# Kernel tuning notes

Hardware: AMD Instinct MI355X
Metric: run time of the kernel (lower is better)

Reference implementation:

```python
import jax, jax.numpy as jnp
import numpy as np
from jax import lax

B, C, H, W = 4, 256, 64, 64
C8 = C // 8


def _conv1x1(x, w, b):
    # x: (B,C,H,W), w: (O,C) -> (B,O,H,W)
    return jnp.einsum('bchw,oc->bohw', x, w) + b[None, :, None, None]


def setup_inputs() -> dict:
    key = jax.random.key(0)
    ks = jax.random.split(key, 9)
    s1 = 1.0 / np.sqrt(C)          # fan-in scale for 1x1 convs
    sf = 1.0 / np.sqrt(2 * C * 9)  # fan-in scale for 3x3 conv
    return {
        'front_x':     jax.random.normal(ks[0], (B, C, H, W), jnp.float32),
        'cross_x':     jax.random.normal(ks[1], (B, C, H, W), jnp.float32),
        'front_x_hat': jax.random.normal(ks[2], (B, C, H, W), jnp.float32),
        'Wq': jax.random.normal(ks[3], (C8, C), jnp.float32) * s1,
        'bq': jnp.zeros((C8,), jnp.float32),
        'Wk': jax.random.normal(ks[4], (C8, C), jnp.float32) * s1,
        'bk': jnp.zeros((C8,), jnp.float32),
        'Wv': jax.random.normal(ks[5], (C, C), jnp.float32) * s1,
        'bv': jnp.zeros((C,), jnp.float32),
        'Wf': jax.random.normal(ks[6], (C, 2 * C, 3, 3), jnp.float32) * sf,
        'bf': jnp.zeros((C,), jnp.float32),
    }


def reference(front_x, cross_x, front_x_hat, Wq, bq, Wk, bk, Wv, bv, Wf, bf):
    b, c, h, w = front_x.shape
    hw = h * w
    # projections -> (B, C/8, HW)
    q = _conv1x1(cross_x, Wq, bq).reshape(b, -1, hw)
    k = _conv1x1(front_x, Wk, bk).reshape(b, -1, hw)
    # energy[b,i,j] = <key_i, query_j>  (B, HW, HW)
    energy = jnp.einsum('bci,bcj->bij', k, q)
    front_star = jnp.max(energy, axis=1)     # (B, HW) best key score per query
    front_arg = jnp.argmax(energy, axis=1)   # (B, HW) best key index per query
    # value projection and hard gather of best-matching value per position
    v = _conv1x1(front_x_hat, Wv, bv).reshape(b, c, hw)
    T = jnp.take_along_axis(v, front_arg[:, None, :], axis=2).reshape(b, c, h, w)
    S = front_star.reshape(b, 1, h, w)
    cat = jnp.concatenate([front_x, T], axis=1)  # (B, 2C, H, W)
    res = lax.conv_general_dilated(
        cat, Wf, window_strides=(1, 1), padding='SAME',
        dimension_numbers=('NCHW', 'OIHW', 'NCHW')) + bf[None, :, None, None]
    return front_x + res * S
```

## Files before the change

### kernel.cpp

```cpp
#include <hip/hip_runtime.h>

#define Bn 4
#define Cn 256
#define C8 32
#define Hn 64
#define Wn 64
#define HWn 4096
#define PADR 80
#define ROWS (HWn + 2 * PADR)
#define MARGIN 6e-3f

typedef __bf16 bf16x8 __attribute__((ext_vector_type(8)));
typedef float floatx4 __attribute__((ext_vector_type(4)));
typedef unsigned short u16x8 __attribute__((ext_vector_type(8)));

__device__ __forceinline__ unsigned short f2bf(float f) {
  union { float f; unsigned int u; } c; c.f = f;
  unsigned int u = c.u;
  return (unsigned short)((u + 0x7FFFu + ((u >> 16) & 1u)) >> 16);
}
__device__ __forceinline__ float bf2f(unsigned short h) {
  union { unsigned int u; float f; } c; c.u = ((unsigned int)h) << 16;
  return c.f;
}
__device__ __forceinline__ void gl_lds16(const void* g, void* l) {
  __builtin_amdgcn_global_load_lds(
      (__attribute__((address_space(1))) void*)(uintptr_t)g,
      (__attribute__((address_space(3))) void*)(uintptr_t)l, 16, 0, 0);
}

__global__ void prep_w(const float* __restrict__ Wq, const float* __restrict__ Wk,
                       const float* __restrict__ Wv, const float* __restrict__ Wf,
                       float* __restrict__ Wqf, float* __restrict__ Wkf,
                       unsigned short* __restrict__ Wvb, unsigned short* __restrict__ Wfb,
                       int* __restrict__ cnt) {
  size_t t = (size_t)blockIdx.x * 256 + threadIdx.x;
  if (t == 0) cnt[0] = 0;
  if (t < 8192) {
    int o = (int)(t / 256), c = (int)(t % 256);
    Wqf[(size_t)c * 32 + o] = Wq[t];
    Wkf[(size_t)c * 32 + o] = Wk[t];
  }
  if (t < 65536) Wvb[t] = f2bf(Wv[t]);
  if (t < (size_t)9 * 256 * 512) {
    int tap = (int)(t / (256 * 512));
    int rem = (int)(t % (256 * 512));
    int o = rem / 512, ci = rem % 512;
    Wfb[t] = f2bf(Wf[((size_t)o * 512 + ci) * 9 + tap]);
  }
}

__global__ __launch_bounds__(1024) void proj_qk(
    const float* __restrict__ cross_x, const float* __restrict__ front_x,
    const float* __restrict__ Wqf, const float* __restrict__ bq,
    const float* __restrict__ Wkf, const float* __restrict__ bk,
    float* __restrict__ qf, float* __restrict__ kf,
    unsigned short* __restrict__ qhi, unsigned short* __restrict__ qlo,
    unsigned short* __restrict__ khi, unsigned short* __restrict__ klo) {
  int tid = threadIdx.x;
  int lane = tid & 63, wv = tid >> 6;
  int slice = wv & 3;
  int chunk = wv >> 2;
  int j = blockIdx.x * 64 + lane;
  int b = blockIdx.y;
  int z = blockIdx.z;
  const float* x = (z == 0) ? cross_x : front_x;
  const float* Wg = (z == 0) ? Wqf : Wkf;
  const float* bd = (z == 0) ? bq : bk;
  float* outp = (z == 0) ? qf : kf;
  unsigned short* hip_ = (z == 0) ? qhi : khi;
  unsigned short* lop_ = (z == 0) ? qlo : klo;
  int o0 = slice * 8;
  int c0 = chunk * 64;

  __shared__ __align__(16) float Wl[8192];
  __shared__ float part[3 * 4 * 8 * 64];

  for (int u = tid; u < 8192; u += 1024) Wl[u] = Wg[u];
  __syncthreads();

  const float* xb = x + (size_t)b * Cn * HWn + j;
  floatx4 a0 = (floatx4)0.0f, a1 = (floatx4)0.0f;
#pragma unroll 16
  for (int c = c0; c < c0 + 64; ++c) {
    float xv = xb[(size_t)c * HWn];
    floatx4 wa = *reinterpret_cast<const floatx4*>(&Wl[c * 32 + o0]);
    floatx4 wb = *reinterpret_cast<const floatx4*>(&Wl[c * 32 + o0 + 4]);
    a0 += wa * xv;
    a1 += wb * xv;
  }
  if (chunk > 0) {
    float* dst = &part[(((chunk - 1) * 4 + slice) * 8) * 64];
#pragma unroll
    for (int o = 0; o < 4; ++o) { dst[o * 64 + lane] = a0[o]; dst[(o + 4) * 64 + lane] = a1[o]; }
  }
  __syncthreads();
  if (chunk != 0) return;
#pragma unroll
  for (int q = 0; q < 3; ++q) {
    const float* src = &part[((q * 4 + slice) * 8) * 64];
#pragma unroll
    for (int o = 0; o < 4; ++o) { a0[o] += src[o * 64 + lane]; a1[o] += src[(o + 4) * 64 + lane]; }
  }
  float acc[8];
#pragma unroll
  for (int o = 0; o < 4; ++o) { acc[o] = a0[o] + bd[o0 + o]; acc[o + 4] = a1[o] + bd[o0 + 4 + o]; }

  float* op = outp + ((size_t)b * HWn + j) * C8 + o0;
  u16x8 hv, lv;
#pragma unroll
  for (int o = 0; o < 8; ++o) {
    op[o] = acc[o];
    unsigned short h = f2bf(acc[o]);
    hv[o] = h;
    lv[o] = f2bf(acc[o] - bf2f(h));
  }
  *reinterpret_cast<u16x8*>(hip_ + ((size_t)b * HWn + j) * C8 + o0) = hv;
  *reinterpret_cast<u16x8*>(lop_ + ((size_t)b * HWn + j) * C8 + o0) = lv;
}

__global__ __launch_bounds__(1024) void energy_approx(
    const unsigned short* __restrict__ khi, const unsigned short* __restrict__ klo,
    const unsigned short* __restrict__ qhi, const unsigned short* __restrict__ qlo,
    float* __restrict__ star, int* __restrict__ argb,
    int* __restrict__ cnt, int* __restrict__ list) {
  int b = blockIdx.y;
  int j0 = blockIdx.x * 32;
  int tid = threadIdx.x;
  int lane = tid & 63, wv = tid >> 6;
  int lm = lane & 15, lq = lane >> 4;

  __shared__ float bv1S[16][32];
  __shared__ int   bi1S[16][32];
  __shared__ float bv2S[16][32];

  bf16x8 qh[2], ql[2];
#pragma unroll
  for (int s = 0; s < 2; ++s) {
    int j = j0 + s * 16 + lm;
    qh[s] = *reinterpret_cast<const bf16x8*>(qhi + ((size_t)b * HWn + j) * 32 + lq * 8);
    ql[s] = *reinterpret_cast<const bf16x8*>(qlo + ((size_t)b * HWn + j) * 32 + lq * 8);
  }
  const unsigned short* kh_base = khi + (size_t)b * HWn * 32 + lq * 8;
  const unsigned short* kl_base = klo + (size_t)b * HWn * 32 + lq * 8;

  float b1[2], b2[2];
#pragma unroll
  for (int s = 0; s < 2; ++s) { b1[s] = -3.0e38f; b2[s] = -3.0e38f; }

  int ibase = wv * 256;
#pragma unroll 4
  for (int it = 0; it < 16; ++it) {
    int i0 = ibase + it * 16;
    bf16x8 ah = *reinterpret_cast<const bf16x8*>(kh_base + (size_t)(i0 + lm) * 32);
    bf16x8 al = *reinterpret_cast<const bf16x8*>(kl_base + (size_t)(i0 + lm) * 32);
#pragma unroll
    for (int s = 0; s < 2; ++s) {
      floatx4 acc = (floatx4)0.0f;
      acc = __builtin_amdgcn_mfma_f32_16x16x32_bf16(ah, qh[s], acc, 0, 0, 0);
      acc = __builtin_amdgcn_mfma_f32_16x16x32_bf16(ah, ql[s], acc, 0, 0, 0);
      acc = __builtin_amdgcn_mfma_f32_16x16x32_bf16(al, qh[s], acc, 0, 0, 0);
#pragma unroll
      for (int r = 0; r < 4; ++r) {
        unsigned code = (unsigned)(it * 4 + r);
        union { float f; unsigned u; } cv; cv.f = acc[r];
        cv.u = (cv.u & ~63u) | code;
        float vp = cv.f;
        b2[s] = __builtin_amdgcn_fmed3f(vp, b1[s], b2[s]);
        b1[s] = fmaxf(b1[s], vp);
      }
    }
  }
  int i1[2];
#pragma unroll
  for (int s = 0; s < 2; ++s) {
    union { float f; unsigned u; } cv; cv.f = b1[s];
    unsigned code = cv.u & 63u;
    i1[s] = ibase + (int)(code >> 2) * 16 + lq * 4 + (int)(code & 3u);
  }
#pragma unroll
  for (int s = 0; s < 2; ++s) {
#pragma unroll
    for (int m = 16; m <= 32; m <<= 1) {
      float ob1 = __shfl_xor(b1[s], m, 64);
      int oi1 = __shfl_xor(i1[s], m, 64);
      float ob2 = __shfl_xor(b2[s], m, 64);
      float c2;
      if (ob1 > b1[s] || (ob1 == b1[s] && oi1 < i1[s])) {
        c2 = fmaxf(b1[s], ob2);
        b1[s] = ob1; i1[s] = oi1;
      } else {
        c2 = fmaxf(ob1, b2[s]);
      }
      b2[s] = c2;
    }
    if (lq == 0) {
      bv1S[wv][s * 16 + lm] = b1[s];
      bi1S[wv][s * 16 + lm] = i1[s];
      bv2S[wv][s * 16 + lm] = b2[s];
    }
  }
  __syncthreads();
  if (tid < 32) {
    float B1 = bv1S[0][tid];
    int I1 = bi1S[0][tid];
    float B2 = bv2S[0][tid];
#pragma unroll
    for (int w = 1; w < 16; ++w) {
      float v1 = bv1S[w][tid];
      int ii = bi1S[w][tid];
      float v2 = bv2S[w][tid];
      if (v1 > B1) { B2 = fmaxf(B1, v2); B1 = v1; I1 = ii; }
      else B2 = fmaxf(B2, v1);
    }
    size_t o = (size_t)b * HWn + j0 + tid;
    union { float f; unsigned u; } cs; cs.f = B1;
    cs.u &= ~63u;
    star[o] = cs.f;
    argb[o] = I1;
    if (B1 - B2 < MARGIN) {
      int slot = atomicAdd(cnt, 1);
      list[slot] = (b << 12) | (j0 + (int)tid);
    }
  }
}

__global__ __launch_bounds__(256) void recheck(
    const float* __restrict__ qf, const float* __restrict__ kf,
    const int* __restrict__ cnt, const int* __restrict__ list,
    float* __restrict__ star, int* __restrict__ argb) {
  __shared__ double bvS[4];
  __shared__ int biS[4];
  int n = cnt[0];
  int tid = threadIdx.x;
  int lane = tid & 63, wv = tid >> 6;
  for (int idx = blockIdx.x; idx < n; idx += gridDim.x) {
    int e = list[idx];
    int b = e >> 12, j = e & 4095;
    const float* qp = qf + ((size_t)b * HWn + j) * 32;
    double qj[32];
#pragma unroll
    for (int o = 0; o < 32; ++o) qj[o] = (double)qp[o];
    double best = -1.0e300;
    int bi = 1 << 30;
    for (int i = tid; i < HWn; i += 256) {
      const float* kp = kf + ((size_t)b * HWn + i) * 32;
      double s = 0.0;
#pragma unroll
      for (int o = 0; o < 32; ++o) s += (double)kp[o] * qj[o];
      if (s > best) { best = s; bi = i; }
    }
#pragma unroll
    for (int m = 1; m < 64; m <<= 1) {
      double ob = __shfl_xor(best, m, 64);
      int oi = __shfl_xor(bi, m, 64);
      if (ob > best || (ob == best && oi < bi)) { best = ob; bi = oi; }
    }
    if (lane == 0) { bvS[wv] = best; biS[wv] = bi; }
    __syncthreads();
    if (tid == 0) {
#pragma unroll
      for (int w = 1; w < 4; ++w) {
        if (bvS[w] > best || (bvS[w] == best && biS[w] < bi)) {
          best = bvS[w]; bi = biS[w];
        }
      }
      star[(size_t)b * HWn + j] = (float)best;
      argb[(size_t)b * HWn + j] = bi;
    }
    __syncthreads();
  }
}

__global__ __launch_bounds__(256) void cat_fx(
    const float* __restrict__ fx, const float* __restrict__ fxh,
    unsigned short* __restrict__ catC, unsigned short* __restrict__ xht) {
  int j0 = blockIdx.x * 64;
  int ci0 = blockIdx.y * 64;
  int b = blockIdx.z >> 1;
  int which = blockIdx.z & 1;
  int tid = threadIdx.x;
  __shared__ unsigned short tile[64][66];

  const float* src = (which == 0) ? fx : fxh;
  for (int u = tid; u < 4096; u += 256) {
    int cl = u >> 6, hw_l = u & 63;
    tile[cl][hw_l] = f2bf(src[((size_t)(b * Cn + ci0 + cl)) * HWn + j0 + hw_l]);
  }
  __syncthreads();
  if (which == 0) {
    for (int u = tid; u < 4096; u += 256) {
      int hw_l = u >> 6, cl = u & 63;
      catC[((size_t)b * ROWS + PADR + j0 + hw_l) * 512 + ci0 + cl] = tile[cl][hw_l];
    }
  } else {
    for (int u = tid; u < 4096; u += 256) {
      int hw_l = u >> 6, cl = u & 63;
      xht[((size_t)b * HWn + j0 + hw_l) * 256 + ci0 + cl] = tile[cl][hw_l];
    }
  }
}

__global__ __launch_bounds__(256) void proj_v_mfma(
    const unsigned short* __restrict__ xht, const unsigned short* __restrict__ Wvb,
    const float* __restrict__ bv, unsigned short* __restrict__ vbf) {
  int m0 = blockIdx.x * 128;
  int o0 = blockIdx.y * 128;
  int b = blockIdx.z;
  int tid = threadIdx.x;
  int lane = tid & 63, wv = tid >> 6;
  int wm = wv >> 1, wn = wv & 1;
  int lm = lane & 15, lq = lane >> 4;

  union SMu {
    struct { unsigned short A[2][128 * 32]; unsigned short B[2][128 * 32]; } st;
    unsigned short TS[128 * 136];
  };
  __shared__ __align__(16) SMu sm;

  floatx4 acc[4][4];
#pragma unroll
  for (int im = 0; im < 4; ++im)
#pragma unroll
    for (int in = 0; in < 4; ++in) acc[im][in] = (floatx4)0.0f;

  const int srow = lane >> 2;
  const int soff = (((lane & 3) ^ ((lane >> 3) & 3)) * 8);
  const int sa = (lq ^ ((lm >> 1) & 3)) * 8;
  const unsigned short* ag = Wvb + (size_t)o0 * 256;
  const unsigned short* bg = xht + ((size_t)b * HWn + m0) * 256;

  auto STAGE = [&](unsigned short* Ab, unsigned short* Bb, int kc) {
#pragma unroll
    for (int i = 0; i < 2; ++i) {
      int r0 = wv * 32 + i * 16;
      gl_lds16(ag + ((size_t)(r0 + srow)) * 256 + kc + soff, &Ab[r0 * 32]);
      gl_lds16(bg + ((size_t)(r0 + srow)) * 256 + kc + soff, &Bb[r0 * 32]);
    }
  };
  auto COMPUTE = [&](const unsigned short* Ab, const unsigned short* Bb) {
    bf16x8 afr[4];
#pragma unroll
    for (int im = 0; im < 4; ++im)
      afr[im] = *reinterpret_cast<const bf16x8*>(
          &Ab[(wm * 64 + im * 16 + lm) * 32 + sa]);
#pragma unroll
    for (int in = 0; in < 4; ++in) {
      bf16x8 bfr = *reinterpret_cast<const bf16x8*>(
          &Bb[(wn * 64 + in * 16 + lm) * 32 + sa]);
#pragma unroll
      for (int im = 0; im < 4; ++im)
        acc[im][in] = __builtin_amdgcn_mfma_f32_16x16x32_bf16(
            afr[im], bfr, acc[im][in], 0, 0, 0);
    }
  };

  STAGE(sm.st.A[0], sm.st.B[0], 0);
  __syncthreads();
  for (int kci = 0; kci < 8; kci += 2) {
    if (kci < 7) STAGE(sm.st.A[1], sm.st.B[1], (kci + 1) * 32);
    COMPUTE(sm.st.A[0], sm.st.B[0]);
    __syncthreads();
    if (kci < 6) STAGE(sm.st.A[0], sm.st.B[0], (kci + 2) * 32);
    COMPUTE(sm.st.A[1], sm.st.B[1]);
    __syncthreads();
  }

#pragma unroll
  for (int in = 0; in < 4; ++in) {
    int pl = wn * 64 + in * 16 + lm;
#pragma unroll
    for (int im = 0; im < 4; ++im) {
#pragma unroll
      for (int r = 0; r < 4; ++r) {
        int ol = wm * 64 + im * 16 + lq * 4 + r;
        sm.TS[pl * 136 + ol] = f2bf(acc[im][in][r] + bv[o0 + ol]);
      }
    }
  }
  __syncthreads();
  for (int idx = tid; idx < 128 * 16; idx += 256) {
    int p = idx >> 4, ch = idx & 15;
    u16x8 val = *reinterpret_cast<const u16x8*>(&sm.TS[p * 136 + ch * 8]);
    *reinterpret_cast<u16x8*>(
        &vbf[((size_t)b * HWn + m0 + p) * 256 + o0 + ch * 8]) = val;
  }
}

__global__ __launch_bounds__(256) void gather_cat(
    const unsigned short* __restrict__ vbf, const int* __restrict__ argb,
    unsigned short* __restrict__ catC) {
  int b = blockIdx.y;
  int tid = threadIdx.x;
  if (blockIdx.x == 16) {
    for (int u = tid; u < 2 * PADR * 512; u += 256) {
      int r = u >> 9;
      int rr = (r < PADR) ? r : (HWn + r);
      catC[((size_t)b * ROWS + rr) * 512 + (u & 511)] = 0;
    }
    return;
  }
  __shared__ int ajS[256];
  int j0 = blockIdx.x * 256;
  ajS[tid] = argb[(size_t)b * HWn + j0 + tid];
  __syncthreads();
#pragma unroll 4
  for (int u = tid; u < 256 * 32; u += 256) {
    int pl = u >> 5, ch = u & 31;
    int aj = ajS[pl];
    u16x8 val = *reinterpret_cast<const u16x8*>(
        &vbf[((size_t)b * HWn + aj) * 256 + ch * 8]);
    *reinterpret_cast<u16x8*>(
        &catC[((size_t)b * ROWS + PADR + j0 + pl) * 512 + 256 + ch * 8]) = val;
  }
}

__global__ __launch_bounds__(256) void conv_mfma(
    const unsigned short* __restrict__ catC, const unsigned short* __restrict__ Wfb,
    const float* __restrict__ fx, const float* __restrict__ bfc,
    const float* __restrict__ star, float* __restrict__ out) {
  int m0 = blockIdx.x * 64;
  int o0 = blockIdx.y * 128;
  int b = blockIdx.z;
  int tid = threadIdx.x;
  int lane = tid & 63;
  int wv = tid >> 6;
  int wm = wv >> 1, wn = wv & 1;
  int lm = lane & 15, lq = lane >> 4;
  const bool edge_first = (wn == 0) && (lm == 0);
  const bool edge_last  = (wn == 1) && (lm == 15);

  __shared__ __align__(16) unsigned short AS[2][3 * 128 * 32];
  __shared__ __align__(16) unsigned short BS[2][80 * 32];

  floatx4 acc[4][2];
#pragma unroll
  for (int im = 0; im < 4; ++im)
#pragma unroll
    for (int in = 0; in < 2; ++in) acc[im][in] = (floatx4)0.0f;

  const int srow = lane >> 2;
  const int soff = (((lane & 3) ^ ((lane >> 3) & 3)) * 8);
  const int sa = (lq ^ ((lm >> 1) & 3)) * 8;
  const unsigned short* catb = catC + ((size_t)b * ROWS + PADR + m0 - 65) * 512;
  const unsigned short* wfo = Wfb + (size_t)o0 * 512;

  auto STAGE = [&](unsigned short* ASb, unsigned short* BSb, int step) {
    int g = step >> 4;
    int kc = (step & 15) * 32;
    if (wv < 3) {
      const unsigned short* at = wfo + (size_t)(g * 3 + wv) * 256 * 512;
#pragma unroll
      for (int s = 0; s < 8; ++s)
        gl_lds16(at + ((size_t)(s * 16 + srow)) * 512 + kc + soff,
                 &ASb[(wv * 128 + s * 16) * 32]);
    } else {
      const unsigned short* bt = catb + (size_t)(g * 64) * 512;
#pragma unroll
      for (int s = 0; s < 5; ++s)
        gl_lds16(bt + ((size_t)(s * 16 + srow)) * 512 + kc + soff,
                 &BSb[(s * 16) * 32]);
    }
  };
  auto COMPUTE = [&](const unsigned short* ASb, const unsigned short* BSb) {
#pragma unroll
    for (int t = 0; t < 3; ++t) {
      bf16x8 afr[4];
#pragma unroll
      for (int im = 0; im < 4; ++im)
        afr[im] = *reinterpret_cast<const bf16x8*>(
            &ASb[(t * 128 + wm * 64 + im * 16 + lm) * 32 + sa]);
#pragma unroll
      for (int in = 0; in < 2; ++in) {
        int u = wn * 32 + in * 16 + lm + t;
        int sb = (lq ^ ((u >> 1) & 3)) * 8;
        u16x8 braw = *reinterpret_cast<const u16x8*>(&BSb[u * 32 + sb]);
        if ((t == 0 && in == 0 && edge_first) ||
            (t == 2 && in == 1 && edge_last))
          braw = (u16x8)(unsigned short)0;
        union { u16x8 u8; bf16x8 h; } cvt; cvt.u8 = braw;
#pragma unroll
        for (int im = 0; im < 4; ++im)
          acc[im][in] = __builtin_amdgcn_mfma_f32_16x16x32_bf16(
              afr[im], cvt.h, acc[im][in], 0, 0, 0);
      }
    }
  };

  STAGE(AS[0], BS[0], 0);
  __syncthreads();
  for (int st = 0; st < 48; st += 2) {
    if (st < 47) STAGE(AS[1], BS[1], st + 1);
    COMPUTE(AS[0], BS[0]);
    __syncthreads();
    if (st < 46) STAGE(AS[0], BS[0], st + 2);
    COMPUTE(AS[1], BS[1]);
    __syncthreads();
  }

#pragma unroll
  for (int in = 0; in < 2; ++in) {
    int p = m0 + wn * 32 + in * 16 + lm;
    float s = star[(size_t)b * HWn + p];
#pragma unroll
    for (int im = 0; im < 4; ++im) {
      int ob = o0 + wm * 64 + im * 16 + lq * 4;
#pragma unroll
      for (int r = 0; r < 4; ++r) {
        size_t idx = ((size_t)(b * Cn + ob + r)) * HWn + p;
        out[idx] = fx[idx] + (acc[im][in][r] + bfc[ob + r]) * s;
      }
    }
  }
}

extern "C" void kernel_launch(void* const* d_in, const int* in_sizes, int n_in,
                              void* d_out, int out_size, void* d_ws, size_t ws_size,
                              hipStream_t stream) {
  const float* front_x   = (const float*)d_in[0];
  const float* cross_x   = (const float*)d_in[1];
  const float* front_hat = (const float*)d_in[2];
  const float* Wq = (const float*)d_in[3];
  const float* bq = (const float*)d_in[4];
  const float* Wk = (const float*)d_in[5];
  const float* bk = (const float*)d_in[6];
  const float* Wv = (const float*)d_in[7];
  const float* bv = (const float*)d_in[8];
  const float* Wf = (const float*)d_in[9];
  const float* bf = (const float*)d_in[10];
  float* out = (float*)d_out;

  char* ws = (char*)d_ws;
  size_t off = 0;
  auto alloc = [&](size_t bytes) -> void* {
    void* p = (void*)(ws + off);
    off += (bytes + 255) & ~(size_t)255;
    return p;
  };
  float* Wqf = (float*)alloc(8192 * sizeof(float));
  float* Wkf = (float*)alloc(8192 * sizeof(float));
  unsigned short* Wvb = (unsigned short*)alloc(65536 * sizeof(unsigned short));
  unsigned short* Wfb = (unsigned short*)alloc((size_t)9 * 256 * 512 * sizeof(unsigned short));
  float* qf  = (float*)alloc((size_t)Bn * HWn * C8 * sizeof(float));
  float* kf  = (float*)alloc((size_t)Bn * HWn * C8 * sizeof(float));
  unsigned short* qhi = (unsigned short*)alloc((size_t)Bn * HWn * C8 * 2);
  unsigned short* qlo = (unsigned short*)alloc((size_t)Bn * HWn * C8 * 2);
  unsigned short* khi = (unsigned short*)alloc((size_t)Bn * HWn * C8 * 2);
  unsigned short* klo = (unsigned short*)alloc((size_t)Bn * HWn * C8 * 2);
  float*  star = (float*)alloc((size_t)Bn * HWn * sizeof(float));
  int*    argb = (int*)alloc((size_t)Bn * HWn * sizeof(int));
  int*    cnt  = (int*)alloc(256);
  int*    list = (int*)alloc((size_t)Bn * HWn * sizeof(int));
  unsigned short* xht = (unsigned short*)alloc((size_t)Bn * HWn * 256 * 2);
  unsigned short* vbf = (unsigned short*)alloc((size_t)Bn * HWn * 256 * 2);
  unsigned short* catC = (unsigned short*)alloc((size_t)Bn * ROWS * 512 * sizeof(unsigned short));

  prep_w<<<dim3((9 * 256 * 512 + 255) / 256), dim3(256), 0, stream>>>(
      Wq, Wk, Wv, Wf, Wqf, Wkf, Wvb, Wfb, cnt);

  proj_qk<<<dim3(HWn / 64, Bn, 2), dim3(1024), 0, stream>>>(
      cross_x, front_x, Wqf, bq, Wkf, bk, qf, kf, qhi, qlo, khi, klo);

  energy_approx<<<dim3(HWn / 32, Bn), dim3(1024), 0, stream>>>(
      khi, klo, qhi, qlo, star, argb, cnt, list);

  recheck<<<dim3(256), dim3(256), 0, stream>>>(qf, kf, cnt, list, star, argb);

  cat_fx<<<dim3(HWn / 64, Cn / 64, Bn * 2), dim3(256), 0, stream>>>(
      front_x, front_hat, catC, xht);

  proj_v_mfma<<<dim3(HWn / 128, Cn / 128, Bn), dim3(256), 0, stream>>>(
      xht, Wvb, bv, vbf);

  gather_cat<<<dim3(HWn / 256 + 1, Bn), dim3(256), 0, stream>>>(vbf, argb, catC);

  conv_mfma<<<dim3(HWn / 64, Cn / 128, Bn), dim3(256), 0, stream>>>(
      catC, Wfb, front_x, bf, star, out);
}
```

Baseline: 244.4 us.

## Enlarge conv tile to 128 pixels and pipeline loads with partial vmcnt waits

```diff
diff --git a/kernel.cpp b/kernel.cpp
--- a/kernel.cpp
+++ b/kernel.cpp
@@ -330,24 +330,24 @@
   const unsigned short* ag = Wvb + (size_t)o0 * 256;
   const unsigned short* bg = xht + ((size_t)b * HWn + m0) * 256;
 
-  auto STAGE = [&](unsigned short* Ab, unsigned short* Bb, int kc) {
+  auto STAGE = [&](int buf, int kc) {
 #pragma unroll
     for (int i = 0; i < 2; ++i) {
       int r0 = wv * 32 + i * 16;
-      gl_lds16(ag + ((size_t)(r0 + srow)) * 256 + kc + soff, &Ab[r0 * 32]);
-      gl_lds16(bg + ((size_t)(r0 + srow)) * 256 + kc + soff, &Bb[r0 * 32]);
+      gl_lds16(ag + ((size_t)(r0 + srow)) * 256 + kc + soff, &sm.st.A[buf][r0 * 32]);
+      gl_lds16(bg + ((size_t)(r0 + srow)) * 256 + kc + soff, &sm.st.B[buf][r0 * 32]);
     }
   };
-  auto COMPUTE = [&](const unsigned short* Ab, const unsigned short* Bb) {
+  auto COMPUTE = [&](int buf) {
     bf16x8 afr[4];
 #pragma unroll
     for (int im = 0; im < 4; ++im)
       afr[im] = *reinterpret_cast<const bf16x8*>(
-          &Ab[(wm * 64 + im * 16 + lm) * 32 + sa]);
+          &sm.st.A[buf][(wm * 64 + im * 16 + lm) * 32 + sa]);
 #pragma unroll
     for (int in = 0; in < 4; ++in) {
       bf16x8 bfr = *reinterpret_cast<const bf16x8*>(
-          &Bb[(wn * 64 + in * 16 + lm) * 32 + sa]);
+          &sm.st.B[buf][(wn * 64 + in * 16 + lm) * 32 + sa]);
 #pragma unroll
       for (int im = 0; im < 4; ++im)
         acc[im][in] = __builtin_amdgcn_mfma_f32_16x16x32_bf16(
@@ -355,16 +355,21 @@
     }
   };
 
-  STAGE(sm.st.A[0], sm.st.B[0], 0);
-  __syncthreads();
-  for (int kci = 0; kci < 8; kci += 2) {
-    if (kci < 7) STAGE(sm.st.A[1], sm.st.B[1], (kci + 1) * 32);
-    COMPUTE(sm.st.A[0], sm.st.B[0]);
-    __syncthreads();
-    if (kci < 6) STAGE(sm.st.A[0], sm.st.B[0], (kci + 2) * 32);
-    COMPUTE(sm.st.A[1], sm.st.B[1]);
-    __syncthreads();
-  }
+  STAGE(0, 0);
+#pragma unroll 2
+  for (int st = 0; st < 8; ++st) {
+    __builtin_amdgcn_s_barrier();
+    if (st < 7) {
+      STAGE((st + 1) & 1, (st + 1) * 32);
+      asm volatile("s_waitcnt vmcnt(4)" ::: "memory");
+    } else {
+      asm volatile("s_waitcnt vmcnt(0)" ::: "memory");
+    }
+    __builtin_amdgcn_s_barrier();
+    __builtin_amdgcn_sched_barrier(0);
+    COMPUTE(st & 1);
+  }
+  __builtin_amdgcn_s_barrier();
 
 #pragma unroll
   for (int in = 0; in < 4; ++in) {
@@ -419,7 +424,7 @@
     const unsigned short* __restrict__ catC, const unsigned short* __restrict__ Wfb,
     const float* __restrict__ fx, const float* __restrict__ bfc,
     const float* __restrict__ star, float* __restrict__ out) {
-  int m0 = blockIdx.x * 64;
+  int m0 = blockIdx.x * 128;
   int o0 = blockIdx.y * 128;
   int b = blockIdx.z;
   int tid = threadIdx.x;
@@ -427,17 +432,17 @@
   int wv = tid >> 6;
   int wm = wv >> 1, wn = wv & 1;
   int lm = lane & 15, lq = lane >> 4;
-  const bool edge_first = (wn == 0) && (lm == 0);
-  const bool edge_last  = (wn == 1) && (lm == 15);
+  const bool lane_first = (lm == 0);
+  const bool lane_last = (lm == 15);
 
   __shared__ __align__(16) unsigned short AS[2][3 * 128 * 32];
-  __shared__ __align__(16) unsigned short BS[2][80 * 32];
-
-  floatx4 acc[4][2];
+  __shared__ __align__(16) unsigned short BS[2][144 * 32];
+
+  floatx4 acc[4][4];
 #pragma unroll
   for (int im = 0; im < 4; ++im)
 #pragma unroll
-    for (int in = 0; in < 2; ++in) acc[im][in] = (floatx4)0.0f;
+    for (int in = 0; in < 4; ++in) acc[im][in] = (floatx4)0.0f;
 
   const int srow = lane >> 2;
   const int soff = (((lane & 3) ^ ((lane >> 3) & 3)) * 8);
@@ -445,7 +450,7 @@
   const unsigned short* catb = catC + ((size_t)b * ROWS + PADR + m0 - 65) * 512;
   const unsigned short* wfo = Wfb + (size_t)o0 * 512;
 
-  auto STAGE = [&](unsigned short* ASb, unsigned short* BSb, int step) {
+  auto STAGE = [&](int buf, int step) {
     int g = step >> 4;
     int kc = (step & 15) * 32;
     if (wv < 3) {
@@ -453,30 +458,30 @@
 #pragma unroll
       for (int s = 0; s < 8; ++s)
         gl_lds16(at + ((size_t)(s * 16 + srow)) * 512 + kc + soff,
-                 &ASb[(wv * 128 + s * 16) * 32]);
+                 &AS[buf][(wv * 128 + s * 16) * 32]);
     } else {
       const unsigned short* bt = catb + (size_t)(g * 64) * 512;
 #pragma unroll
-      for (int s = 0; s < 5; ++s)
+      for (int s = 0; s < 9; ++s)
         gl_lds16(bt + ((size_t)(s * 16 + srow)) * 512 + kc + soff,
-                 &BSb[(s * 16) * 32]);
+                 &BS[buf][(s * 16) * 32]);
     }
   };
-  auto COMPUTE = [&](const unsigned short* ASb, const unsigned short* BSb) {
+  auto COMPUTE = [&](int buf) {
 #pragma unroll
     for (int t = 0; t < 3; ++t) {
       bf16x8 afr[4];
 #pragma unroll
       for (int im = 0; im < 4; ++im)
         afr[im] = *reinterpret_cast<const bf16x8*>(
-            &ASb[(t * 128 + wm * 64 + im * 16 + lm) * 32 + sa]);
-#pragma unroll
-      for (int in = 0; in < 2; ++in) {
-        int u = wn * 32 + in * 16 + lm + t;
+            &AS[buf][(t * 128 + wm * 64 + im * 16 + lm) * 32 + sa]);
+#pragma unroll
+      for (int in = 0; in < 4; ++in) {
+        int u = wn * 64 + in * 16 + lm + t;
         int sb = (lq ^ ((u >> 1) & 3)) * 8;
-        u16x8 braw = *reinterpret_cast<const u16x8*>(&BSb[u * 32 + sb]);
-        if ((t == 0 && in == 0 && edge_first) ||
-            (t == 2 && in == 1 && edge_last))
+        u16x8 braw = *reinterpret_cast<const u16x8*>(&BS[buf][u * 32 + sb]);
+        if ((t == 0 && in == 0 && lane_first) ||
+            (t == 2 && in == 3 && lane_last))
           braw = (u16x8)(unsigned short)0;
         union { u16x8 u8; bf16x8 h; } cvt; cvt.u8 = braw;
 #pragma unroll
@@ -487,20 +492,25 @@
     }
   };
 
-  STAGE(AS[0], BS[0], 0);
-  __syncthreads();
-  for (int st = 0; st < 48; st += 2) {
-    if (st < 47) STAGE(AS[1], BS[1], st + 1);
-    COMPUTE(AS[0], BS[0]);
-    __syncthreads();
-    if (st < 46) STAGE(AS[0], BS[0], st + 2);
-    COMPUTE(AS[1], BS[1]);
-    __syncthreads();
-  }
-
-#pragma unroll
-  for (int in = 0; in < 2; ++in) {
-    int p = m0 + wn * 32 + in * 16 + lm;
+  STAGE(0, 0);
+#pragma unroll 2
+  for (int st = 0; st < 48; ++st) {
+    __builtin_amdgcn_s_barrier();
+    if (st < 47) {
+      STAGE((st + 1) & 1, st + 1);
+      if (wv < 3) asm volatile("s_waitcnt vmcnt(8)" ::: "memory");
+      else        asm volatile("s_waitcnt vmcnt(9)" ::: "memory");
+    } else {
+      asm volatile("s_waitcnt vmcnt(0)" ::: "memory");
+    }
+    __builtin_amdgcn_s_barrier();
+    __builtin_amdgcn_sched_barrier(0);
+    COMPUTE(st & 1);
+  }
+
+#pragma unroll
+  for (int in = 0; in < 4; ++in) {
+    int p = m0 + wn * 64 + in * 16 + lm;
     float s = star[(size_t)b * HWn + p];
 #pragma unroll
     for (int im = 0; im < 4; ++im) {
@@ -574,6 +584,6 @@
 
   gather_cat<<<dim3(HWn / 256 + 1, Bn), dim3(256), 0, stream>>>(vbf, argb, catC);
 
-  conv_mfma<<<dim3(HWn / 64, Cn / 128, Bn), dim3(256), 0, stream>>>(
+  conv_mfma<<<dim3(HWn / 128, Cn / 128, Bn), dim3(256), 0, stream>>>(
       catC, Wfb, front_x, bf, star, out);
 }
```

Result: no change. 241.8 us (-1.1%).
